# Kernel optimization log

Measured on AMD Instinct MI355X. Metric: run time of the kernel, lower is better.

The kernel has to match this reference:

```python
import jax, jax.numpy as jnp
import numpy as np

D_MODEL = 128
N_HEADS = 8
D_K = D_MODEL // N_HEADS
N_NODES = 50000
N_EDGES = 800000


def setup_inputs() -> dict:
    key = jax.random.key(0)
    ks = jax.random.split(key, 8)
    X = jax.random.normal(ks[0], (N_NODES, D_MODEL), dtype=jnp.float32)
    nbr_src = jax.random.randint(ks[1], (N_EDGES,), 0, N_NODES, dtype=jnp.int32)
    nbr_dst = jax.random.randint(ks[2], (N_EDGES,), 0, N_NODES, dtype=jnp.int32)
    s = 1.0 / np.sqrt(D_MODEL)
    W_qkv = jax.random.normal(ks[3], (3 * D_MODEL, D_MODEL), dtype=jnp.float32) * s
    w_bias = jax.random.normal(ks[4], (N_HEADS, D_MODEL), dtype=jnp.float32) * s
    W_gate = jax.random.normal(ks[5], (D_MODEL, D_MODEL), dtype=jnp.float32) * s
    b_gate = jax.random.normal(ks[6], (D_MODEL,), dtype=jnp.float32) * s
    W_o = jax.random.normal(ks[7], (D_MODEL, D_MODEL), dtype=jnp.float32) * s
    return {"X": X, "W_qkv": W_qkv, "w_bias": w_bias, "W_gate": W_gate,
            "b_gate": b_gate, "W_o": W_o, "nbr_src": nbr_src,
            "nbr_dst": nbr_dst, "num_cells": N_NODES}


def segment_softmax(scores, seg, num_segments):
    # scores: [E, H], seg: [E] -> softmax over edges sharing the same seg id
    mx = jax.ops.segment_max(scores, seg, num_segments=num_segments)  # [N, H]
    mx = jnp.where(jnp.isfinite(mx), mx, -1e9)
    exp_s = jnp.exp(scores - mx[seg])
    sm = jax.ops.segment_sum(exp_s, seg, num_segments=num_segments)  # [N, H]
    return exp_s / (sm[seg] + 1e-12)


def reference(X, W_qkv, w_bias, W_gate, b_gate, W_o, nbr_src, nbr_dst, num_cells):
    H, dk = N_HEADS, D_K
    scale = 1.0 / np.sqrt(dk)
    qkv = (X @ W_qkv.T).reshape(-1, 3, H, dk)      # [N, 3, H, dk]
    Q, K, V = qkv[:, 0], qkv[:, 1], qkv[:, 2]
    gate = jax.nn.sigmoid(X @ W_gate.T + b_gate).reshape(-1, H, dk)
    bias = X @ w_bias.T                             # [N, H]
    scores = jnp.einsum('ehd,ehd->eh', Q[nbr_src], K[nbr_dst]) * scale + bias[nbr_src]
    attn = segment_softmax(scores, nbr_src, num_cells)          # [E, H]
    out = jax.ops.segment_sum(attn[:, :, None] * V[nbr_dst], nbr_src,
                              num_segments=num_cells)           # [N, H, dk]
    return (gate * out).reshape(-1, D_MODEL) @ W_o.T
```

## Files before the change

kernel.cpp:

```cpp
#include <hip/hip_runtime.h>
#include <hip/hip_fp16.h>

#define DM 128
#define NHEADS 8
#define MAXDEG 64
#define SROW 136

typedef _Float16 half8 __attribute__((ext_vector_type(8)));
typedef _Float16 half2v __attribute__((ext_vector_type(2)));
typedef float floatx4 __attribute__((ext_vector_type(4)));

union H8 { half8 v; half2v h2[4]; };

__device__ __forceinline__ half8 cvt_h8(float4 f0, float4 f1) {
  return half8{(_Float16)f0.x, (_Float16)f0.y, (_Float16)f0.z, (_Float16)f0.w,
               (_Float16)f1.x, (_Float16)f1.y, (_Float16)f1.z, (_Float16)f1.w};
}

__global__ __launch_bounds__(256) void proj_csr(
    const float* __restrict__ X, const float* __restrict__ Wqkv,
    const float* __restrict__ Wgate, const float* __restrict__ wbias,
    const float* __restrict__ b_gate,
    const int* __restrict__ nsrc, const int* __restrict__ ndst,
    int* __restrict__ cnt, unsigned short* __restrict__ csr_dst,
    _Float16* __restrict__ Q, _Float16* __restrict__ KV,
    _Float16* __restrict__ gate, float* __restrict__ bias,
    int M, int E, int P) {
  __shared__ _Float16 As[64 * SROW];
  __shared__ _Float16 Bs[64 * SROW];
  int tid = threadIdx.x;
  int bid = blockIdx.x;

  if (bid >= P) {
    int ebase = (bid - P) * 8192;
    for (int g = 0; g < 4; g++) {
      int s[8], d[8];
#pragma unroll
      for (int j = 0; j < 8; j++) {
        int e = ebase + (g * 8 + j) * 256 + tid;
        s[j] = (e < E) ? __builtin_nontemporal_load(nsrc + e) : -1;
        d[j] = (e < E) ? __builtin_nontemporal_load(ndst + e) : 0;
      }
#pragma unroll
      for (int j = 0; j < 8; j++) {
        if (s[j] >= 0) {
          int p = atomicAdd(&cnt[s[j]], 1);
          if (p < MAXDEG) csr_dst[(size_t)s[j] * MAXDEG + p] = (unsigned short)d[j];
        }
      }
    }
    return;
  }

  int m0 = bid * 64;

#pragma unroll
  for (int i = 0; i < 2; i++) {
    int u = tid + i * 256;
    int r = u >> 3;
    int cc = (u & 7) * 16;
    int gr = m0 + r;
    float4 f0, f1, f2, f3;
    if (gr < M) {
      const float4* src = (const float4*)(X + (size_t)gr * 128 + cc);
      f0 = src[0]; f1 = src[1]; f2 = src[2]; f3 = src[3];
    } else {
      f0 = f1 = f2 = f3 = make_float4(0.f, 0.f, 0.f, 0.f);
    }
    *(half8*)(As + r * SROW + cc) = cvt_h8(f0, f1);
    *(half8*)(As + r * SROW + cc + 8) = cvt_h8(f2, f3);
  }

  int wid = tid >> 6, lane = tid & 63;
  int quad = lane >> 4, l16 = lane & 15;
  int mw = wid * 16;

  for (int c = 0; c < 9; c++) {
    __syncthreads();
#pragma unroll
    for (int i = 0; i < 4; i++) {
      int u = tid + i * 256;
      int r = u >> 4;
      int cc = (u & 15) * 8;
      int grow = c * 64 + r;
      const float* src = nullptr;
      if (grow < 384)      src = Wqkv + (size_t)grow * 128 + cc;
      else if (grow < 512) src = Wgate + (size_t)(grow - 384) * 128 + cc;
      else if (grow < 520) src = wbias + (size_t)(grow - 512) * 128 + cc;
      half8 h = {};
      if (src) {
        float4 f0 = ((const float4*)src)[0];
        float4 f1 = ((const float4*)src)[1];
        h = cvt_h8(f0, f1);
      }
      *(half8*)(Bs + r * SROW + cc) = h;
    }
    __syncthreads();

    floatx4 acc[4] = {};
#pragma unroll
    for (int kc = 0; kc < 4; kc++) {
      int ko = kc * 32 + quad * 8;
      half8 a0 = *(const half8*)(As + (mw + l16) * SROW + ko);
      half8 b[4];
#pragma unroll
      for (int ni = 0; ni < 4; ni++)
        b[ni] = *(const half8*)(Bs + (ni * 16 + l16) * SROW + ko);
#pragma unroll
      for (int ni = 0; ni < 4; ni++)
        acc[ni] = __builtin_amdgcn_mfma_f32_16x16x32_f16(a0, b[ni], acc[ni], 0, 0, 0);
    }

    if (c == 8) {
      if (l16 < 8) {
#pragma unroll
        for (int r = 0; r < 4; r++) {
          int row = m0 + mw + quad * 4 + r;
          if (row < M) bias[(size_t)row * 8 + l16] = acc[0][r];
        }
      }
    } else {
      int reg = c >> 1;
#pragma unroll
      for (int ni = 0; ni < 4; ni++) {
        int colL = (c & 1) * 64 + ni * 16 + l16;
#pragma unroll
        for (int r = 0; r < 4; r++) {
          int row = m0 + mw + quad * 4 + r;
          if (row >= M) continue;
          float v = acc[ni][r];
          if (reg == 0)      Q[(size_t)row * 128 + colL] = (_Float16)v;
          else if (reg == 1) KV[(size_t)row * 256 + colL] = (_Float16)v;
          else if (reg == 2) KV[(size_t)row * 256 + 128 + colL] = (_Float16)v;
          else gate[(size_t)row * 128 + colL] =
                 (_Float16)(1.0f / (1.0f + __expf(-(v + b_gate[colL]))));
        }
      }
    }
  }
}

__global__ __launch_bounds__(256) void final_gemm_mfma(
    const _Float16* __restrict__ A, const float* __restrict__ Wo,
    float* __restrict__ C, int M) {
  __shared__ _Float16 As[128 * SROW];
  __shared__ _Float16 Bs[64 * SROW];
  int tid = threadIdx.x;
  int m0 = blockIdx.x * 128, n0 = blockIdx.y * 64;
#pragma unroll
  for (int i = 0; i < 8; i++) {
    int u = tid + i * 256;
    int r = u >> 4;
    int cc = (u & 15) * 8;
    int gr = m0 + r;
    int4 val = make_int4(0, 0, 0, 0);
    if (gr < M) val = *(const int4*)(A + (size_t)gr * 128 + cc);
    *(int4*)(As + r * SROW + cc) = val;
  }
#pragma unroll
  for (int i = 0; i < 4; i++) {
    int u = tid + i * 256;
    int r = u >> 4;
    int cc = (u & 15) * 8;
    const float* src = Wo + (size_t)(n0 + r) * 128 + cc;
    float4 f0 = ((const float4*)src)[0];
    float4 f1 = ((const float4*)src)[1];
    *(half8*)(Bs + r * SROW + cc) = cvt_h8(f0, f1);
  }
  __syncthreads();

  int wid = tid >> 6, lane = tid & 63;
  int quad = lane >> 4, l16 = lane & 15;
  int mw = (wid >> 1) * 64;
  int nw = (wid & 1) * 32;

  floatx4 acc[4][2] = {};
#pragma unroll
  for (int kc = 0; kc < 4; kc++) {
    int ko = kc * 32 + quad * 8;
    half8 a[4], b[2];
#pragma unroll
    for (int mi = 0; mi < 4; mi++)
      a[mi] = *(const half8*)(As + (mw + mi * 16 + l16) * SROW + ko);
#pragma unroll
    for (int ni = 0; ni < 2; ni++)
      b[ni] = *(const half8*)(Bs + (nw + ni * 16 + l16) * SROW + ko);
#pragma unroll
    for (int mi = 0; mi < 4; mi++)
#pragma unroll
      for (int ni = 0; ni < 2; ni++)
        acc[mi][ni] = __builtin_amdgcn_mfma_f32_16x16x32_f16(a[mi], b[ni], acc[mi][ni], 0, 0, 0);
  }
#pragma unroll
  for (int mi = 0; mi < 4; mi++) {
#pragma unroll
    for (int ni = 0; ni < 2; ni++) {
      int col = n0 + nw + ni * 16 + l16;
#pragma unroll
      for (int r = 0; r < 4; r++) {
        int row = m0 + mw + mi * 16 + quad * 4 + r;
        if (row >= M) continue;
        C[(size_t)row * 128 + col] = acc[mi][ni][r];
      }
    }
  }
}

__global__ __launch_bounds__(256) void attn_fused(
    const int* __restrict__ cnt, const unsigned short* __restrict__ csr_dst,
    const _Float16* __restrict__ Q, const _Float16* __restrict__ KV,
    const float* __restrict__ bias, const _Float16* __restrict__ gate,
    _Float16* __restrict__ gated, int N) {
  int wave = threadIdx.x >> 6, lane = threadIdx.x & 63;
  int n = blockIdx.x * 4 + wave;
  if (n >= N) return;
  int deg = __builtin_nontemporal_load(cnt + n);
  if (deg > MAXDEG) deg = MAXDEG;
  int qtr = lane >> 4, l16 = lane & 15;
  int ch0 = l16 * 8;

  int dstv = (int)__builtin_nontemporal_load(csr_dst + (size_t)n * MAXDEG + lane);

  H8 qu; qu.v = __builtin_nontemporal_load((const half8*)(Q + (size_t)n * DM + ch0));
  float bias_h = __builtin_nontemporal_load(bias + (size_t)n * NHEADS + (l16 >> 1));

  float acc[8] = {};
  float den = 0.f;
  int iters = (deg + 3) >> 2;

  H8 kb[4], vb[4];
  bool bb[4];
#pragma unroll
  for (int j = 0; j < 4; j++) {
    bb[j] = false;
    kb[j].v = half8{}; vb[j].v = half8{};
    if (j < iters) {
      int e = j * 4 + qtr;
      bb[j] = e < deg;
      int d = __shfl(dstv, e);
      d = bb[j] ? d : 0;
      const _Float16* kvp = KV + (size_t)d * 256 + ch0;
      kb[j].v = *(const half8*)kvp;
      vb[j].v = *(const half8*)(kvp + 128);
    }
  }

  for (int base = 0; base < iters; base += 4) {
#pragma unroll
    for (int j = 0; j < 4; j++) {
      float p = 0.f;
#pragma unroll
      for (int t = 0; t < 4; t++)
        p = __builtin_amdgcn_fdot2(qu.h2[t], kb[j].h2[t], p, false);
      p += __shfl_xor(p, 1);
      float w = __expf(p * 0.25f + bias_h);
      if (!bb[j]) w = 0.f;
      den += w;
#pragma unroll
      for (int t = 0; t < 8; t++) acc[t] = fmaf(w, (float)vb[j].v[t], acc[t]);
      int idx = base + 4 + j;
      bb[j] = false;
      if (idx < iters) {
        int e = idx * 4 + qtr;
        bb[j] = e < deg;
        int d = __shfl(dstv, e);
        d = bb[j] ? d : 0;
        const _Float16* kvp = KV + (size_t)d * 256 + ch0;
        kb[j].v = *(const half8*)kvp;
        vb[j].v = *(const half8*)(kvp + 128);
      }
    }
  }

#pragma unroll
  for (int j = 0; j < 8; j++) acc[j] += __shfl_xor(acc[j], 16);
#pragma unroll
  for (int j = 0; j < 8; j++) acc[j] += __shfl_xor(acc[j], 32);
  den += __shfl_xor(den, 16);
  den += __shfl_xor(den, 32);

  if (qtr == 0) {
    float inv = 1.0f / (den + 1e-12f);
    half8 gv = __builtin_nontemporal_load((const half8*)(gate + (size_t)n * DM + ch0));
    half8 o;
#pragma unroll
    for (int j = 0; j < 8; j++) o[j] = (_Float16)(acc[j] * inv * (float)gv[j]);
    *(half8*)(gated + (size_t)n * DM + ch0) = o;
  }
}

extern "C" void kernel_launch(void* const* d_in, const int* in_sizes, int n_in,
                              void* d_out, int out_size, void* d_ws, size_t ws_size,
                              hipStream_t stream) {
  const float* X     = (const float*)d_in[0];
  const float* Wqkv  = (const float*)d_in[1];
  const float* wbias = (const float*)d_in[2];
  const float* Wgate = (const float*)d_in[3];
  const float* bgate = (const float*)d_in[4];
  const float* Wo    = (const float*)d_in[5];
  const int*   nsrc  = (const int*)d_in[6];
  const int*   ndst  = (const int*)d_in[7];
  int N = in_sizes[0] / 128;
  int E = in_sizes[6];
  float* out = (float*)d_out;

  char* p = (char*)d_ws;
  _Float16* Q16     = (_Float16*)p; p += (size_t)N * 128 * sizeof(_Float16);
  _Float16* KV16    = (_Float16*)p; p += (size_t)N * 256 * sizeof(_Float16);
  _Float16* gate16  = (_Float16*)p; p += (size_t)N * 128 * sizeof(_Float16);
  _Float16* gated16 = (_Float16*)p; p += (size_t)N * 128 * sizeof(_Float16);
  float* bias       = (float*)p;    p += (size_t)N * 8 * sizeof(float);
  int* cnt          = (int*)p;      p += (size_t)N * sizeof(int);
  unsigned short* csr_dst = (unsigned short*)p;
  p += (size_t)N * MAXDEG * sizeof(unsigned short);

  hipMemsetAsync(cnt, 0, (size_t)N * sizeof(int), stream);

  int P = (N + 63) / 64;
  int C = (E + 8191) / 8192;
  proj_csr<<<P + C, 256, 0, stream>>>(X, Wqkv, Wgate, wbias, bgate, nsrc, ndst,
                                      cnt, csr_dst, Q16, KV16, gate16, bias, N, E, P);

  attn_fused<<<(N + 3) / 4, 256, 0, stream>>>(cnt, csr_dst, Q16, KV16, bias,
                                              gate16, gated16, N);

  dim3 fg((N + 127) / 128, 2);
  final_gemm_mfma<<<fg, 256, 0, stream>>>(gated16, Wo, out, N);
}
```

Before: 233.8 us.

## Fuse output projection into attention kernel and split CSR build into own kernel

The final W_o GEMM is folded into the attention kernel: each block converts all of W_o to fp16 in LDS, writes each node's gated output to LDS, and computes the 128-wide output row with fdot2 instructions. This removes the gated intermediate buffer round trip and one kernel launch. In exchange every attention block (only 4 nodes) reloads and converts the full 128x128 W_o, uses about 34KB of LDS, which may cap occupancy, and runs the projection on scalar dot products instead of MFMA. Separately, the CSR build moves out of the projection kernel into its own launch with smaller 2048-edge blocks, which serializes it ahead of the projection GEMM.

```diff
diff --git a/kernel.cpp b/kernel.cpp
--- a/kernel.cpp
+++ b/kernel.cpp
@@ -5,8 +5,10 @@
 #define NHEADS 8
 #define MAXDEG 64
 #define SROW 136
+#define WSTRIDE 132
 
 typedef _Float16 half8 __attribute__((ext_vector_type(8)));
+typedef _Float16 half4 __attribute__((ext_vector_type(4)));
 typedef _Float16 half2v __attribute__((ext_vector_type(2)));
 typedef float floatx4 __attribute__((ext_vector_type(4)));
 
@@ -17,42 +19,37 @@
                (_Float16)f1.x, (_Float16)f1.y, (_Float16)f1.z, (_Float16)f1.w};
 }
 
-__global__ __launch_bounds__(256) void proj_csr(
+__global__ __launch_bounds__(256) void csr_build(
+    const int* __restrict__ nsrc, const int* __restrict__ ndst,
+    int* __restrict__ cnt, unsigned short* __restrict__ csr_dst, int E) {
+  int tid = threadIdx.x;
+  int ebase = blockIdx.x * 2048;
+  int s[8], d[8];
+#pragma unroll
+  for (int j = 0; j < 8; j++) {
+    int e = ebase + j * 256 + tid;
+    s[j] = (e < E) ? __builtin_nontemporal_load(nsrc + e) : -1;
+    d[j] = (e < E) ? __builtin_nontemporal_load(ndst + e) : 0;
+  }
+#pragma unroll
+  for (int j = 0; j < 8; j++) {
+    if (s[j] >= 0) {
+      int p = atomicAdd(&cnt[s[j]], 1);
+      if (p < MAXDEG) csr_dst[(size_t)s[j] * MAXDEG + p] = (unsigned short)d[j];
+    }
+  }
+}
+
+__global__ __launch_bounds__(256) void proj_gemm(
     const float* __restrict__ X, const float* __restrict__ Wqkv,
     const float* __restrict__ Wgate, const float* __restrict__ wbias,
     const float* __restrict__ b_gate,
-    const int* __restrict__ nsrc, const int* __restrict__ ndst,
-    int* __restrict__ cnt, unsigned short* __restrict__ csr_dst,
     _Float16* __restrict__ Q, _Float16* __restrict__ KV,
-    _Float16* __restrict__ gate, float* __restrict__ bias,
-    int M, int E, int P) {
+    _Float16* __restrict__ gate, float* __restrict__ bias, int M) {
   __shared__ _Float16 As[64 * SROW];
   __shared__ _Float16 Bs[64 * SROW];
   int tid = threadIdx.x;
-  int bid = blockIdx.x;
-
-  if (bid >= P) {
-    int ebase = (bid - P) * 8192;
-    for (int g = 0; g < 4; g++) {
-      int s[8], d[8];
-#pragma unroll
-      for (int j = 0; j < 8; j++) {
-        int e = ebase + (g * 8 + j) * 256 + tid;
-        s[j] = (e < E) ? __builtin_nontemporal_load(nsrc + e) : -1;
-        d[j] = (e < E) ? __builtin_nontemporal_load(ndst + e) : 0;
-      }
-#pragma unroll
-      for (int j = 0; j < 8; j++) {
-        if (s[j] >= 0) {
-          int p = atomicAdd(&cnt[s[j]], 1);
-          if (p < MAXDEG) csr_dst[(size_t)s[j] * MAXDEG + p] = (unsigned short)d[j];
-        }
-      }
-    }
-    return;
-  }
-
-  int m0 = bid * 64;
+  int m0 = blockIdx.x * 64;
 
 #pragma unroll
   for (int i = 0; i < 2; i++) {
@@ -140,89 +137,40 @@
   }
 }
 
-__global__ __launch_bounds__(256) void final_gemm_mfma(
-    const _Float16* __restrict__ A, const float* __restrict__ Wo,
-    float* __restrict__ C, int M) {
-  __shared__ _Float16 As[128 * SROW];
-  __shared__ _Float16 Bs[64 * SROW];
-  int tid = threadIdx.x;
-  int m0 = blockIdx.x * 128, n0 = blockIdx.y * 64;
-#pragma unroll
-  for (int i = 0; i < 8; i++) {
-    int u = tid + i * 256;
-    int r = u >> 4;
-    int cc = (u & 15) * 8;
-    int gr = m0 + r;
-    int4 val = make_int4(0, 0, 0, 0);
-    if (gr < M) val = *(const int4*)(A + (size_t)gr * 128 + cc);
-    *(int4*)(As + r * SROW + cc) = val;
-  }
-#pragma unroll
-  for (int i = 0; i < 4; i++) {
-    int u = tid + i * 256;
-    int r = u >> 4;
-    int cc = (u & 15) * 8;
-    const float* src = Wo + (size_t)(n0 + r) * 128 + cc;
-    float4 f0 = ((const float4*)src)[0];
-    float4 f1 = ((const float4*)src)[1];
-    *(half8*)(Bs + r * SROW + cc) = cvt_h8(f0, f1);
-  }
-  __syncthreads();
-
-  int wid = tid >> 6, lane = tid & 63;
-  int quad = lane >> 4, l16 = lane & 15;
-  int mw = (wid >> 1) * 64;
-  int nw = (wid & 1) * 32;
-
-  floatx4 acc[4][2] = {};
-#pragma unroll
-  for (int kc = 0; kc < 4; kc++) {
-    int ko = kc * 32 + quad * 8;
-    half8 a[4], b[2];
-#pragma unroll
-    for (int mi = 0; mi < 4; mi++)
-      a[mi] = *(const half8*)(As + (mw + mi * 16 + l16) * SROW + ko);
-#pragma unroll
-    for (int ni = 0; ni < 2; ni++)
-      b[ni] = *(const half8*)(Bs + (nw + ni * 16 + l16) * SROW + ko);
-#pragma unroll
-    for (int mi = 0; mi < 4; mi++)
-#pragma unroll
-      for (int ni = 0; ni < 2; ni++)
-        acc[mi][ni] = __builtin_amdgcn_mfma_f32_16x16x32_f16(a[mi], b[ni], acc[mi][ni], 0, 0, 0);
-  }
-#pragma unroll
-  for (int mi = 0; mi < 4; mi++) {
-#pragma unroll
-    for (int ni = 0; ni < 2; ni++) {
-      int col = n0 + nw + ni * 16 + l16;
-#pragma unroll
-      for (int r = 0; r < 4; r++) {
-        int row = m0 + mw + mi * 16 + quad * 4 + r;
-        if (row >= M) continue;
-        C[(size_t)row * 128 + col] = acc[mi][ni][r];
-      }
-    }
-  }
-}
-
 __global__ __launch_bounds__(256) void attn_fused(
     const int* __restrict__ cnt, const unsigned short* __restrict__ csr_dst,
     const _Float16* __restrict__ Q, const _Float16* __restrict__ KV,
     const float* __restrict__ bias, const _Float16* __restrict__ gate,
-    _Float16* __restrict__ gated, int N) {
-  int wave = threadIdx.x >> 6, lane = threadIdx.x & 63;
+    const float* __restrict__ Wo, float* __restrict__ out, int N) {
+  __shared__ _Float16 WoLds[128 * WSTRIDE];
+  __shared__ _Float16 gLds[4 * 128];
+  int tid = threadIdx.x;
+
+  {
+    int r = tid >> 1, cc = (tid & 1) * 64;
+    const float* wrow = Wo + (size_t)r * 128 + cc;
+#pragma unroll
+    for (int i = 0; i < 16; i++) {
+      float4 f = ((const float4*)wrow)[i];
+      half4 h = {(_Float16)f.x, (_Float16)f.y, (_Float16)f.z, (_Float16)f.w};
+      *(half4*)(WoLds + r * WSTRIDE + cc + i * 4) = h;
+    }
+  }
+  __syncthreads();
+
+  int wave = tid >> 6, lane = tid & 63;
   int n = blockIdx.x * 4 + wave;
-  if (n >= N) return;
-  int deg = __builtin_nontemporal_load(cnt + n);
+  bool active = n < N;
+  int nn = active ? n : 0;
+  int deg = active ? __builtin_nontemporal_load(cnt + nn) : 0;
   if (deg > MAXDEG) deg = MAXDEG;
   int qtr = lane >> 4, l16 = lane & 15;
   int ch0 = l16 * 8;
 
-  int dstv = (int)__builtin_nontemporal_load(csr_dst + (size_t)n * MAXDEG + lane);
-
-  H8 qu; qu.v = __builtin_nontemporal_load((const half8*)(Q + (size_t)n * DM + ch0));
-  float bias_h = __builtin_nontemporal_load(bias + (size_t)n * NHEADS + (l16 >> 1));
+  int dstv = (int)__builtin_nontemporal_load(csr_dst + (size_t)nn * MAXDEG + lane);
+
+  H8 qu; qu.v = __builtin_nontemporal_load((const half8*)(Q + (size_t)nn * DM + ch0));
+  float bias_h = __builtin_nontemporal_load(bias + (size_t)nn * NHEADS + (l16 >> 1));
 
   float acc[8] = {};
   float den = 0.f;
@@ -281,11 +229,32 @@
 
   if (qtr == 0) {
     float inv = 1.0f / (den + 1e-12f);
-    half8 gv = __builtin_nontemporal_load((const half8*)(gate + (size_t)n * DM + ch0));
+    half8 gv = __builtin_nontemporal_load((const half8*)(gate + (size_t)nn * DM + ch0));
     half8 o;
 #pragma unroll
     for (int j = 0; j < 8; j++) o[j] = (_Float16)(acc[j] * inv * (float)gv[j]);
-    *(half8*)(gated + (size_t)n * DM + ch0) = o;
+    *(half8*)(gLds + wave * 128 + ch0) = o;
+  }
+  __syncthreads();
+
+  float o1 = 0.f, o2 = 0.f;
+  const _Float16* gbase = gLds + wave * 128;
+  const _Float16* w1base = WoLds + (size_t)lane * WSTRIDE;
+  const _Float16* w2base = WoLds + (size_t)(lane + 64) * WSTRIDE;
+#pragma unroll
+  for (int k4 = 0; k4 < 32; k4++) {
+    half4 g  = *(const half4*)(gbase + k4 * 4);
+    half4 w1 = *(const half4*)(w1base + k4 * 4);
+    half4 w2 = *(const half4*)(w2base + k4 * 4);
+    half2v g0 = {g[0], g[1]}, g1 = {g[2], g[3]};
+    o1 = __builtin_amdgcn_fdot2(g0, half2v{w1[0], w1[1]}, o1, false);
+    o1 = __builtin_amdgcn_fdot2(g1, half2v{w1[2], w1[3]}, o1, false);
+    o2 = __builtin_amdgcn_fdot2(g0, half2v{w2[0], w2[1]}, o2, false);
+    o2 = __builtin_amdgcn_fdot2(g1, half2v{w2[2], w2[3]}, o2, false);
+  }
+  if (active) {
+    out[(size_t)n * 128 + lane] = o1;
+    out[(size_t)n * 128 + lane + 64] = o2;
   }
 }
 
@@ -308,7 +277,6 @@
   _Float16* Q16     = (_Float16*)p; p += (size_t)N * 128 * sizeof(_Float16);
   _Float16* KV16    = (_Float16*)p; p += (size_t)N * 256 * sizeof(_Float16);
   _Float16* gate16  = (_Float16*)p; p += (size_t)N * 128 * sizeof(_Float16);
-  _Float16* gated16 = (_Float16*)p; p += (size_t)N * 128 * sizeof(_Float16);
   float* bias       = (float*)p;    p += (size_t)N * 8 * sizeof(float);
   int* cnt          = (int*)p;      p += (size_t)N * sizeof(int);
   unsigned short* csr_dst = (unsigned short*)p;
@@ -316,14 +284,13 @@
 
   hipMemsetAsync(cnt, 0, (size_t)N * sizeof(int), stream);
 
+  int C = (E + 2047) / 2048;
+  csr_build<<<C, 256, 0, stream>>>(nsrc, ndst, cnt, csr_dst, E);
+
   int P = (N + 63) / 64;
-  int C = (E + 8191) / 8192;
-  proj_csr<<<P + C, 256, 0, stream>>>(X, Wqkv, Wgate, wbias, bgate, nsrc, ndst,
-                                      cnt, csr_dst, Q16, KV16, gate16, bias, N, E, P);
+  proj_gemm<<<P, 256, 0, stream>>>(X, Wqkv, Wgate, wbias, bgate,
+                                   Q16, KV16, gate16, bias, N);
 
   attn_fused<<<(N + 3) / 4, 256, 0, stream>>>(cnt, csr_dst, Q16, KV16, bias,
-                                              gate16, gated16, N);
-
-  dim3 fg((N + 127) / 128, 2);
-  final_gemm_mfma<<<fg, 256, 0, stream>>>(gated16, Wo, out, N);
-}
+                                              gate16, Wo, out, N);
+}
```

Result: slower. 297.5 us (+27.2%).
